# Kernel tuning notes

Measured on AMD Instinct MI355X. Metric: run time of the kernel, lower is better.

The kernel has to match this reference:

```python
import jax, jax.numpy as jnp
import numpy as np

NODE_DIM = 256
EDGE_IN = 128
EDGE_OUT = 128
BIAS_DIM = NODE_DIM // 2          # node_dilation = 2
HIDDEN = BIAS_DIM * 2 + EDGE_IN   # 384
B, N = 1, 512


def setup_inputs() -> dict:
    key = jax.random.key(0)
    ks = jax.random.split(key, 12)
    s = lambda fi, fo: 1.0 / np.sqrt(fi)
    return {
        "node_embed": jax.random.normal(ks[0], (B, N, NODE_DIM), jnp.float32),
        "edge_embed": jax.random.normal(ks[1], (B, N, N, EDGE_IN), jnp.float32),
        "w_init": jax.random.normal(ks[2], (NODE_DIM, BIAS_DIM), jnp.float32) * s(NODE_DIM, BIAS_DIM),
        "b_init": jnp.zeros((BIAS_DIM,), jnp.float32),
        "w_t0": jax.random.normal(ks[3], (HIDDEN, HIDDEN), jnp.float32) * s(HIDDEN, HIDDEN),
        "b_t0": jnp.zeros((HIDDEN,), jnp.float32),
        "w_t1": jax.random.normal(ks[4], (HIDDEN, HIDDEN), jnp.float32) * s(HIDDEN, HIDDEN),
        "b_t1": jnp.zeros((HIDDEN,), jnp.float32),
        "w_fin": jax.random.normal(ks[5], (HIDDEN, EDGE_OUT), jnp.float32) * 0.02,
        "b_fin": jnp.zeros((EDGE_OUT,), jnp.float32),
        "ln_g": jnp.ones((EDGE_OUT,), jnp.float32),
        "ln_b": jnp.zeros((EDGE_OUT,), jnp.float32),
    }


def _layer_norm(x, g, b, eps=1e-5):
    mu = jnp.mean(x, axis=-1, keepdims=True)
    var = jnp.mean(jnp.square(x - mu), axis=-1, keepdims=True)
    return (x - mu) * jax.lax.rsqrt(var + eps) * g + b


def reference(node_embed, edge_embed, w_init, b_init, w_t0, b_t0, w_t1, b_t1,
              w_fin, b_fin, ln_g, ln_b):
    b, n, _ = node_embed.shape
    # initial node projection: [B, N, BIAS_DIM]
    nb = node_embed @ w_init + b_init
    # edge_bias = concat(tile over j, tile over i): [B, N, N, 2*BIAS_DIM]
    bias_i = jnp.broadcast_to(nb[:, :, None, :], (b, n, n, nb.shape[-1]))
    bias_j = jnp.broadcast_to(nb[:, None, :, :], (b, n, n, nb.shape[-1]))
    h = jnp.concatenate([edge_embed, bias_i, bias_j], axis=-1)  # [B,N,N,HIDDEN]
    t = jax.nn.relu(h @ w_t0 + b_t0)
    t = jax.nn.relu(t @ w_t1 + b_t1)
    # residual + final linear + LayerNorm
    out = (t + h) @ w_fin + b_fin
    return _layer_norm(out, ln_g, ln_b)
```

## Files before the change

### kernel.cpp

```cpp
#include <hip/hip_runtime.h>


typedef short sv8 __attribute__((ext_vector_type(8)));
typedef float f32x4 __attribute__((ext_vector_type(4)));

union F8U { float4 v4[2]; float f[8]; };

__device__ __forceinline__ void async_cp16(const void* g, void* l) {
  __builtin_amdgcn_global_load_lds(
      (const __attribute__((address_space(1))) void*)g,
      (__attribute__((address_space(3))) void*)l, 16, 0, 0);
}

__device__ __forceinline__ void split8(const float* v, sv8& hi, sv8& lo) {
#pragma unroll
  for (int i = 0; i < 8; i++) {
    unsigned u = __float_as_uint(v[i]);
    hi[i] = (short)(u >> 16);
    float fl = v[i] - __uint_as_float(u & 0xFFFF0000u);
    lo[i] = (short)(__float_as_uint(fl) >> 16);
  }
}

__global__ void node_proj(const float* __restrict__ node,
                          const float* __restrict__ w,
                          const float* __restrict__ b,
                          float* __restrict__ nb) {
  __shared__ float sn[256];
  int i = blockIdx.x;
  int t = threadIdx.x;
  sn[t] = node[i * 256 + t];
  sn[t + 128] = node[i * 256 + t + 128];
  __syncthreads();
  float acc = b[t];
  for (int k = 0; k < 256; k++) acc += sn[k] * w[k * 128 + t];
  nb[i * 128 + t] = acc;
}

__global__ void pq_proj(const float* __restrict__ nb,
                        const float* __restrict__ w0,
                        const float* __restrict__ b0,
                        float* __restrict__ Pb, float* __restrict__ Qm) {
  __shared__ float sn[128];
  const int j = blockIdx.x, t = threadIdx.x;
  if (t < 128) sn[t] = nb[j * 128 + t];
  __syncthreads();
  float ap = b0[t], aq = 0.0f;
  for (int k = 0; k < 128; k++) {
    const float nk = sn[k];
    ap += nk * w0[(128 + k) * 384 + t];
    aq += nk * w0[(256 + k) * 384 + t];
  }
  Pb[j * 384 + t] = ap;
  Qm[j * 384 + t] = aq;
}

__global__ void pack_b(const float* __restrict__ W, int N, int NKT,
                       float* __restrict__ dst) {
  const int nt = blockIdx.x, kt = blockIdx.y, l = threadIdx.x;
  const int n = nt * 16 + (l & 15);
  const int k0 = kt * 32 + ((l >> 4) * 8);
  float v[8];
#pragma unroll
  for (int i = 0; i < 8; i++) v[i] = W[(size_t)(k0 + i) * N + n];
  sv8 hi, lo;
  split8(v, hi, lo);
  char* base = (char*)dst + (size_t)((nt * NKT + kt) * 2) * 1024;
  *(sv8*)(base + l * 16) = hi;
  *(sv8*)(base + 1024 + l * 16) = lo;
}

__device__ __forceinline__ void stage_e(const float* E, long mblk, int kt,
                                        char* dst, int wid, int lane) {
#pragma unroll
  for (int q = 0; q < 2; q++) {
    int c = wid * 2 + q;
    int row = c * 8 + (lane >> 3);
    int kb = ((lane & 7) * 16) ^ ((row & 7) << 4);
    const char* src =
        (const char*)E + (size_t)(mblk + row) * 512 + (size_t)kt * 128 + kb;
    async_cp16(src, dst + c * 1024);
  }
}

template <int PW>
__device__ __forceinline__ void stage_apk(const float* Apk, long mt0, int NKT,
                                          int kt, char* dst, int wid,
                                          int lane) {
#pragma unroll
  for (int q = 0; q < PW; q++) {
    int idx = wid * PW + q;
    int mt = idx >> 1, sp = idx & 1;
    const char* src = (const char*)Apk +
                      (size_t)(((mt0 + mt) * NKT + kt) * 2 + sp) * 1024 +
                      lane * 16;
    async_cp16(src, dst + idx * 1024);
  }
}

template <int PW>
__device__ __forceinline__ void stage_bpk(const float* Bpk, int NKT, int kt,
                                          char* dst, int wid, int lane) {
#pragma unroll
  for (int q = 0; q < PW; q++) {
    int idx = wid * PW + q;
    int nt = idx >> 1, sp = idx & 1;
    const char* src = (const char*)Bpk +
                      (size_t)((nt * NKT + kt) * 2 + sp) * 1024 + lane * 16;
    async_cp16(src, dst + idx * 1024);
  }
}

#define MFMA __builtin_amdgcn_mfma_f32_16x16x32_bf16

__global__ __launch_bounds__(512, 2) void gemm0_k(
    const float* __restrict__ E, const float* __restrict__ W0pk,
    const float* __restrict__ Pb, const float* __restrict__ Qm,
    float* __restrict__ C0pk, long m0) {
  __shared__ __align__(16) char sm[135168];
  const int t = threadIdx.x, lane = t & 63, wid = t >> 6;
  const int rb = wid >> 2, cb = wid & 3;
  const long mblk = m0 + (long)blockIdx.x * 128;
  const int i_node = (int)(mblk >> 9);
  float* sPb = (float*)(sm + 131072);
  if (t < 96)
    *(float4*)(sPb + t * 4) = *(const float4*)(Pb + i_node * 384 + t * 4);

  f32x4 acc[4][6] = {};

  stage_e(E, mblk, 0, sm, wid, lane);
  stage_bpk<6>(W0pk, 4, 0, sm + 32768, wid, lane);
  __syncthreads();

  for (int kt = 0; kt < 4; kt++) {
    const int buf = kt & 1;
    if (kt < 3) {
      stage_e(E, mblk, kt + 1, sm + (buf ^ 1) * 16384, wid, lane);
      stage_bpk<6>(W0pk, 4, kt + 1, sm + 32768 + (buf ^ 1) * 49152, wid, lane);
    }
    const char* sA = sm + buf * 16384;
    const char* sB = sm + 32768 + buf * 49152;
    sv8 ah[4], al[4], bh[6], bl[6];
#pragma unroll
    for (int rt = 0; rt < 4; rt++) {
      int row = rb * 64 + rt * 16 + (lane & 15);
      int c0 = (lane >> 4) * 32;
      F8U v;
      v.v4[0] = *(const float4*)(sA + row * 128 + (c0 ^ ((row & 7) << 4)));
      v.v4[1] =
          *(const float4*)(sA + row * 128 + ((c0 + 16) ^ ((row & 7) << 4)));
      split8(v.f, ah[rt], al[rt]);
    }
#pragma unroll
    for (int nt = 0; nt < 6; nt++) {
      int gnt = cb * 6 + nt;
      bh[nt] = *(const sv8*)(sB + gnt * 2048 + lane * 16);
      bl[nt] = *(const sv8*)(sB + gnt * 2048 + 1024 + lane * 16);
    }
#pragma unroll
    for (int rt = 0; rt < 4; rt++)
#pragma unroll
      for (int nt = 0; nt < 6; nt++) {
        acc[rt][nt] = MFMA(ah[rt], bh[nt], acc[rt][nt], 0, 0, 0);
        acc[rt][nt] = MFMA(ah[rt], bl[nt], acc[rt][nt], 0, 0, 0);
        acc[rt][nt] = MFMA(al[rt], bh[nt], acc[rt][nt], 0, 0, 0);
      }
    __syncthreads();
  }

  float* scr = (float*)(sm + wid * 16384);
  const long mrow0 = mblk + rb * 64;
#pragma unroll
  for (int h = 0; h < 2; h++) {
#pragma unroll
    for (int rt = 0; rt < 4; rt++)
#pragma unroll
      for (int ntl = 0; ntl < 3; ntl++) {
        int nt = h * 3 + ntl;
#pragma unroll
        for (int rg = 0; rg < 4; rg++) {
          int row = rt * 16 + (lane >> 4) * 4 + rg;
          scr[row * 52 + ntl * 16 + (lane & 15)] = acc[rt][nt][rg];
        }
      }
#pragma unroll
    for (int q = 0; q < 6; q++) {
      const int row = lane;
      const int colg = cb * 96 + h * 48 + q * 8;
      F8U v;
      v.v4[0] = *(float4*)(scr + row * 52 + q * 8);
      v.v4[1] = *(float4*)(scr + row * 52 + q * 8 + 4);
      const long m = mrow0 + row;
      const int j = (int)(m & 511);
      F8U qv;
      qv.v4[0] = *(const float4*)(Qm + (size_t)j * 384 + colg);
      qv.v4[1] = *(const float4*)(Qm + (size_t)j * 384 + colg + 4);
#pragma unroll
      for (int i = 0; i < 8; i++)
        v.f[i] = fmaxf(v.f[i] + sPb[colg + i] + qv.f[i], 0.0f);
      sv8 hi, lo;
      split8(v.f, hi, lo);
      const int rowb = rb * 64 + row;
      const long mt = (long)blockIdx.x * 8 + (rowb >> 4);
      const int lane2 = (rowb & 15) | (((colg >> 3) & 3) << 4);
      char* base = (char*)C0pk + (size_t)((mt * 12 + (colg >> 5)) * 2) * 1024;
      *(sv8*)(base + lane2 * 16) = hi;
      *(sv8*)(base + 1024 + lane2 * 16) = lo;
    }
  }
}

__global__ __launch_bounds__(512, 2) void gemm1_k(
    const float* __restrict__ C0pk, const float* __restrict__ W1pk,
    const float* __restrict__ b1, const float* __restrict__ E,
    const float* __restrict__ nb, float* __restrict__ A2pk, long m0) {
  __shared__ __align__(16) char sm[135168];
  const int t = threadIdx.x, lane = t & 63, wid = t >> 6;
  const int rb = wid >> 2, cb = wid & 3;
  const long mblk = m0 + (long)blockIdx.x * 128;
  const int i_node = (int)(mblk >> 9);
  float* sB1 = (float*)(sm + 131072);
  float* snbi = (float*)(sm + 131072 + 1536);
  if (t < 96) *(float4*)(sB1 + t * 4) = *(const float4*)(b1 + t * 4);
  if (t < 32)
    *(float4*)(snbi + t * 4) = *(const float4*)(nb + i_node * 128 + t * 4);

  f32x4 acc[4][6] = {};

  const long mt0 = (long)blockIdx.x * 8;
  stage_apk<2>(C0pk, mt0, 12, 0, sm, wid, lane);
  stage_bpk<6>(W1pk, 12, 0, sm + 32768, wid, lane);
  __syncthreads();

  for (int kt = 0; kt < 12; kt++) {
    const int buf = kt & 1;
    if (kt < 11) {
      stage_apk<2>(C0pk, mt0, 12, kt + 1, sm + (buf ^ 1) * 16384, wid, lane);
      stage_bpk<6>(W1pk, 12, kt + 1, sm + 32768 + (buf ^ 1) * 49152, wid,
                   lane);
    }
    const char* sA = sm + buf * 16384;
    const char* sB = sm + 32768 + buf * 49152;
    sv8 ah[4], al[4], bh[6], bl[6];
#pragma unroll
    for (int rt = 0; rt < 4; rt++) {
      int mtl = rb * 4 + rt;
      ah[rt] = *(const sv8*)(sA + mtl * 2048 + lane * 16);
      al[rt] = *(const sv8*)(sA + mtl * 2048 + 1024 + lane * 16);
    }
#pragma unroll
    for (int nt = 0; nt < 6; nt++) {
      int gnt = cb * 6 + nt;
      bh[nt] = *(const sv8*)(sB + gnt * 2048 + lane * 16);
      bl[nt] = *(const sv8*)(sB + gnt * 2048 + 1024 + lane * 16);
    }
#pragma unroll
    for (int rt = 0; rt < 4; rt++)
#pragma unroll
      for (int nt = 0; nt < 6; nt++) {
        acc[rt][nt] = MFMA(ah[rt], bh[nt], acc[rt][nt], 0, 0, 0);
        acc[rt][nt] = MFMA(ah[rt], bl[nt], acc[rt][nt], 0, 0, 0);
        acc[rt][nt] = MFMA(al[rt], bh[nt], acc[rt][nt], 0, 0, 0);
      }
    __syncthreads();
  }

  float* scr = (float*)(sm + wid * 16384);
  const long mrow0 = mblk + rb * 64;
#pragma unroll
  for (int h = 0; h < 2; h++) {
#pragma unroll
    for (int rt = 0; rt < 4; rt++)
#pragma unroll
      for (int ntl = 0; ntl < 3; ntl++) {
        int nt = h * 3 + ntl;
#pragma unroll
        for (int rg = 0; rg < 4; rg++) {
          int row = rt * 16 + (lane >> 4) * 4 + rg;
          scr[row * 52 + ntl * 16 + (lane & 15)] = acc[rt][nt][rg];
        }
      }
#pragma unroll
    for (int q = 0; q < 6; q++) {
      const int row = lane;
      const int colg = cb * 96 + h * 48 + q * 8;
      F8U v;
      v.v4[0] = *(float4*)(scr + row * 52 + q * 8);
      v.v4[1] = *(float4*)(scr + row * 52 + q * 8 + 4);
      const long m = mrow0 + row;
      const int j = (int)(m & 511);
      F8U hv;
      if (colg < 128) {
        hv.v4[0] = *(const float4*)(E + (size_t)m * 128 + colg);
        hv.v4[1] = *(const float4*)(E + (size_t)m * 128 + colg + 4);
      } else if (colg < 256) {
        hv.v4[0] = *(const float4*)(snbi + (colg - 128));
        hv.v4[1] = *(const float4*)(snbi + (colg - 128) + 4);
      } else {
        hv.v4[0] = *(const float4*)(nb + (size_t)j * 128 + (colg - 256));
        hv.v4[1] = *(const float4*)(nb + (size_t)j * 128 + (colg - 256) + 4);
      }
#pragma unroll
      for (int i = 0; i < 8; i++)
        v.f[i] = fmaxf(v.f[i] + sB1[colg + i], 0.0f) + hv.f[i];
      sv8 hi, lo;
      split8(v.f, hi, lo);
      const int rowb = rb * 64 + row;
      const long mt = (long)blockIdx.x * 8 + (rowb >> 4);
      const int lane2 = (rowb & 15) | (((colg >> 3) & 3) << 4);
      char* base = (char*)A2pk + (size_t)((mt * 12 + (colg >> 5)) * 2) * 1024;
      *(sv8*)(base + lane2 * 16) = hi;
      *(sv8*)(base + 1024 + lane2 * 16) = lo;
    }
  }
}

__global__ __launch_bounds__(256, 1) void gemmF_k(
    const float* __restrict__ A2pk, const float* __restrict__ Wfpk,
    const float* __restrict__ bfin, const float* __restrict__ lng,
    const float* __restrict__ lnb, float* __restrict__ out, long m0) {
  __shared__ __align__(16) char sm[135168];
  const int t = threadIdx.x, lane = t & 63, wid = t >> 6;
  const int rb = wid >> 1, cb = wid & 1;
  const long mblk = m0 + (long)blockIdx.x * 128;
  float* rep = (float*)(sm + 65536);
  float* sG = (float*)(sm + 133120);
  float* sB = sG + 128;
  float* sBf = sG + 256;
  if (t < 128) {
    sG[t] = lng[t];
    sB[t] = lnb[t];
    sBf[t] = bfin[t];
  }

  f32x4 acc[4][4] = {};
  const long mt0 = (long)blockIdx.x * 8;
  stage_apk<4>(A2pk, mt0, 12, 0, sm, wid, lane);
  stage_bpk<4>(Wfpk, 12, 0, sm + 32768, wid, lane);
  __syncthreads();

  for (int kt = 0; kt < 12; kt++) {
    const int buf = kt & 1;
    if (kt < 11) {
      stage_apk<4>(A2pk, mt0, 12, kt + 1, sm + (buf ^ 1) * 16384, wid, lane);
      stage_bpk<4>(Wfpk, 12, kt + 1, sm + 32768 + (buf ^ 1) * 16384, wid,
                   lane);
    }
    const char* sA = sm + buf * 16384;
    const char* sBt = sm + 32768 + buf * 16384;
    sv8 ah[4], al[4], bh[4], bl[4];
#pragma unroll
    for (int rt = 0; rt < 4; rt++) {
      int mtl = rb * 4 + rt;
      ah[rt] = *(const sv8*)(sA + mtl * 2048 + lane * 16);
      al[rt] = *(const sv8*)(sA + mtl * 2048 + 1024 + lane * 16);
    }
#pragma unroll
    for (int nt = 0; nt < 4; nt++) {
      int gnt = cb * 4 + nt;
      bh[nt] = *(const sv8*)(sBt + gnt * 2048 + lane * 16);
      bl[nt] = *(const sv8*)(sBt + gnt * 2048 + 1024 + lane * 16);
    }
#pragma unroll
    for (int rt = 0; rt < 4; rt++)
#pragma unroll
      for (int nt = 0; nt < 4; nt++) {
        acc[rt][nt] = MFMA(ah[rt], bh[nt], acc[rt][nt], 0, 0, 0);
        acc[rt][nt] = MFMA(ah[rt], bl[nt], acc[rt][nt], 0, 0, 0);
        acc[rt][nt] = MFMA(al[rt], bh[nt], acc[rt][nt], 0, 0, 0);
      }
    __syncthreads();
  }

#pragma unroll
  for (int rt = 0; rt < 4; rt++)
#pragma unroll
    for (int nt = 0; nt < 4; nt++)
#pragma unroll
      for (int rg = 0; rg < 4; rg++) {
        int row = rb * 64 + rt * 16 + (lane >> 4) * 4 + rg;
        int col = cb * 64 + nt * 16 + (lane & 15);
        rep[row * 132 + col] = acc[rt][nt][rg] + sBf[col];
      }
  __syncthreads();

  {
    const int row = t >> 1, hf = t & 1;
    float* rp = rep + row * 132 + hf * 64;
    float s = 0.0f, qq = 0.0f;
#pragma unroll
    for (int q = 0; q < 16; q++) {
      float4 v = *(float4*)(rp + q * 4);
      s += v.x + v.y + v.z + v.w;
      qq += v.x * v.x + v.y * v.y + v.z * v.z + v.w * v.w;
    }
    s += __shfl_xor(s, 1);
    qq += __shfl_xor(qq, 1);
    const float mu = s * (1.0f / 128.0f);
    const float var = qq * (1.0f / 128.0f) - mu * mu;
    const float rstd = rsqrtf(var + 1e-5f);
    float* op = out + (size_t)(mblk + row) * 128 + hf * 64;
#pragma unroll
    for (int q = 0; q < 16; q++) {
      float4 v = *(float4*)(rp + q * 4);
      const int c = hf * 64 + q * 4;
      float4 o;
      o.x = (v.x - mu) * rstd * sG[c + 0] + sB[c + 0];
      o.y = (v.y - mu) * rstd * sG[c + 1] + sB[c + 1];
      o.z = (v.z - mu) * rstd * sG[c + 2] + sB[c + 2];
      o.w = (v.w - mu) * rstd * sG[c + 3] + sB[c + 3];
      *(float4*)(op + q * 4) = o;
    }
  }
}

#define ROWS 32
#define PF 388
#define TM 8
union F4 { float4 v; float f[4]; };
union F2 { float2 v; float f[2]; };

__device__ __forceinline__ void stage_tile7(const float* __restrict__ g,
                                            float* l, int nchunk, int t) {
  const int lane = t & 63, wid = t >> 6;
  for (int c = wid; c < nchunk; c += 8)
    async_cp16(g + c * 256 + lane * 4, l + c * 256);
}

__device__ __forceinline__ void trunk_tile7(const float* __restrict__ src,
                                            int koff,
                                            const float* __restrict__ wt,
                                            int cA, int cB, int mr,
                                            float acc[TM][3]) {
  for (int kk = 0; kk < 16; kk += 4) {
    F4 a[TM];
#pragma unroll
    for (int r = 0; r < TM; r++)
      a[r].v = *(const float4*)(src + (mr + r) * PF + koff + kk);
#pragma unroll
    for (int ks = 0; ks < 4; ks++) {
      const float* wrow = wt + (kk + ks) * 384;
      F2 w2;
      w2.v = *(const float2*)(wrow + cA);
      const float w1 = wrow[cB];
#pragma unroll
      for (int r = 0; r < TM; r++) {
        const float ak = a[r].f[ks];
        acc[r][0] += ak * w2.f[0];
        acc[r][1] += ak * w2.f[1];
        acc[r][2] += ak * w1;
      }
    }
  }
}

__global__ __launch_bounds__(512, 1) void edge_fused_r7(
    const float* __restrict__ edge, const float* __restrict__ nbf,
    const float* __restrict__ Pb, const float* __restrict__ Qm,
    const float* __restrict__ w0, const float* __restrict__ w1,
    const float* __restrict__ b1v, const float* __restrict__ wf,
    const float* __restrict__ bfin, const float* __restrict__ lng,
    const float* __restrict__ lnb, float* __restrict__ out) {
  __shared__ __align__(16) float Abuf[ROWS * PF];
  __shared__ __align__(16) float Bbuf[ROWS * PF];
  __shared__ __align__(16) float Wt[2][16 * 384];
  __shared__ __align__(16) float snbi[128];

  const int t = threadIdx.x;
  const int ct = t & 63;
  const int g = t >> 8;
  const int mr = ((t >> 6) & 3) * TM;
  const int cA = g * 192 + 2 * ct;
  const int cB = g * 192 + 128 + ct;
  const int r0 = blockIdx.x * ROWS;
  const int i_node = r0 >> 9, j0 = r0 & 511;

  {
    const int row = t >> 4, q = t & 15;
    const float* ep = edge + (size_t)(r0 + row) * 128 + q * 8;
    float* ap = Abuf + row * PF + q * 8;
    *(float4*)(ap + 0) = *(const float4*)(ep + 0);
    *(float4*)(ap + 4) = *(const float4*)(ep + 4);
  }
  if (t < 32)
    *(float4*)(snbi + t * 4) = *(const float4*)(nbf + i_node * 128 + t * 4);

  stage_tile7(w0, Wt[0], 24, t);

  float acc[TM][3];
  {
    const float* pr = Pb + i_node * 384;
    F2 p2;
    p2.v = *(const float2*)(pr + cA);
    const float p1 = pr[cB];
#pragma unroll
    for (int r = 0; r < TM; r++) {
      const float* qr = Qm + (size_t)(j0 + mr + r) * 384;
      F2 q2;
      q2.v = *(const float2*)(qr + cA);
      acc[r][0] = p2.f[0] + q2.f[0];
      acc[r][1] = p2.f[1] + q2.f[1];
      acc[r][2] = p1 + qr[cB];
    }
  }

  for (int kt = 0; kt < 8; kt++) {
    __syncthreads();
    if (kt < 7) stage_tile7(w0 + (kt + 1) * 6144, Wt[(kt + 1) & 1], 24, t);
    trunk_tile7(Abuf, kt * 16, Wt[kt & 1], cA, cB, mr, acc);
  }

  stage_tile7(w1, Wt[0], 24, t);
#pragma unroll
  for (int r = 0; r < TM; r++) {
    float* dr = Bbuf + (mr + r) * PF;
    F2 e2;
    e2.f[0] = fmaxf(acc[r][0], 0.0f);
    e2.f[1] = fmaxf(acc[r][1], 0.0f);
    *(float2*)(dr + cA) = e2.v;
    dr[cB] = fmaxf(acc[r][2], 0.0f);
  }

  {
    F2 c2;
    c2.v = *(const float2*)(b1v + cA);
    const float c1 = b1v[cB];
#pragma unroll
    for (int r = 0; r < TM; r++) {
      acc[r][0] = c2.f[0];
      acc[r][1] = c2.f[1];
      acc[r][2] = c1;
    }
  }

  for (int kt = 0; kt < 24; kt++) {
    __syncthreads();
    if (kt < 23) stage_tile7(w1 + (kt + 1) * 6144, Wt[(kt + 1) & 1], 24, t);
    trunk_tile7(Bbuf, kt * 16, Wt[kt & 1], cA, cB, mr, acc);
  }

  stage_tile7(wf, Wt[0], 16, t);

#pragma unroll
  for (int r = 0; r < TM; r++) {
    const int row = mr + r;
    float* dr = Abuf + row * PF;
    const float* njr = nbf + (size_t)(j0 + row) * 128;
#pragma unroll
    for (int c = 0; c < 2; c++) {
      const int col = cA + c;
      const float hv = (col < 128) ? dr[col]
                     : (col < 256) ? snbi[col - 128]
                                   : njr[col - 256];
      dr[col] = fmaxf(acc[r][c], 0.0f) + hv;
    }
    {
      const float hv = (cB < 128) ? dr[cB]
                     : (cB < 256) ? snbi[cB - 128]
                                  : njr[cB - 256];
      dr[cB] = fmaxf(acc[r][2], 0.0f) + hv;
    }
  }

  const int mrF = (t >> 6) * 4;
  float af[4][2];
  {
    F2 b2;
    b2.v = *(const float2*)(bfin + ct * 2);
#pragma unroll
    for (int r = 0; r < 4; r++) {
      af[r][0] = b2.f[0];
      af[r][1] = b2.f[1];
    }
  }
  for (int ft = 0; ft < 12; ft++) {
    __syncthreads();
    if (ft < 11) stage_tile7(wf + (ft + 1) * 4096, Wt[(ft + 1) & 1], 16, t);
    const float* wtc = Wt[ft & 1] + ct * 2;
    const int koff = ft * 32;
    for (int kk = 0; kk < 32; kk += 4) {
      F4 a[4];
#pragma unroll
      for (int r = 0; r < 4; r++)
        a[r].v = *(const float4*)(Abuf + (mrF + r) * PF + koff + kk);
#pragma unroll
      for (int ks = 0; ks < 4; ks++) {
        F2 wv;
        wv.v = *(const float2*)(wtc + (kk + ks) * 128);
#pragma unroll
        for (int r = 0; r < 4; r++) {
          const float ak = a[r].f[ks];
          af[r][0] += ak * wv.f[0];
          af[r][1] += ak * wv.f[1];
        }
      }
    }
  }

  {
    F2 g2, bb2;
    g2.v = *(const float2*)(lng + ct * 2);
    bb2.v = *(const float2*)(lnb + ct * 2);
#pragma unroll
    for (int r = 0; r < 4; r++) {
      float s = af[r][0] + af[r][1];
      float q = af[r][0] * af[r][0] + af[r][1] * af[r][1];
#pragma unroll
      for (int off = 1; off <= 32; off <<= 1) {
        s += __shfl_xor(s, off);
        q += __shfl_xor(q, off);
      }
      const float mu = s * (1.0f / 128.0f);
      const float var = q * (1.0f / 128.0f) - mu * mu;
      const float rstd = rsqrtf(var + 1e-5f);
      F2 o;
      o.f[0] = (af[r][0] - mu) * rstd * g2.f[0] + bb2.f[0];
      o.f[1] = (af[r][1] - mu) * rstd * g2.f[1] + bb2.f[1];
      *(float2*)(out + (size_t)(r0 + mrF + r) * 128 + ct * 2) = o.v;
    }
  }
}

extern "C" void kernel_launch(void* const* d_in, const int* in_sizes, int n_in,
                              void* d_out, int out_size, void* d_ws,
                              size_t ws_size, hipStream_t stream) {
  const float* node   = (const float*)d_in[0];
  const float* edge   = (const float*)d_in[1];
  const float* w_init = (const float*)d_in[2];
  const float* b_init = (const float*)d_in[3];
  const float* w_t0   = (const float*)d_in[4];
  const float* b_t0   = (const float*)d_in[5];
  const float* w_t1   = (const float*)d_in[6];
  const float* b_t1   = (const float*)d_in[7];
  const float* w_fin  = (const float*)d_in[8];
  const float* b_fin  = (const float*)d_in[9];
  const float* ln_g   = (const float*)d_in[10];
  const float* ln_b   = (const float*)d_in[11];
  float* out = (float*)d_out;
  float* ws = (float*)d_ws;

  float* nbw  = ws;
  float* Pb   = ws + 65536;
  float* Qm   = ws + 262144;
  float* W0pk = ws + 458752;
  float* W1pk = ws + 507904;
  float* Wfpk = ws + 655360;
  float* C0pk = ws + 704512;

  node_proj<<<512, 128, 0, stream>>>(node, w_init, b_init, nbw);
  pq_proj<<<512, 384, 0, stream>>>(nbw, w_t0, b_t0, Pb, Qm);

  int S = 0;
  long stripe_rows = 0;
  for (int s = 8; s <= 256; s *= 2) {
    long sr = 262144L / s;
    size_t need = (704512ull + 2ull * (size_t)sr * 384ull) * 4ull;
    if (need <= ws_size) { S = s; stripe_rows = sr; break; }
  }

  if (S == 0) {
    edge_fused_r7<<<8192, 512, 0, stream>>>(edge, nbw, Pb, Qm, w_t0, w_t1,
                                            b_t1, w_fin, b_fin, ln_g, ln_b,
                                            out);
    return;
  }

  float* A2pk = C0pk + (size_t)stripe_rows * 384;
  const int blocks = (int)(stripe_rows / 128);

  pack_b<<<dim3(24, 4), 64, 0, stream>>>(w_t0, 384, 4, W0pk);
  pack_b<<<dim3(24, 12), 64, 0, stream>>>(w_t1, 384, 12, W1pk);
  pack_b<<<dim3(8, 12), 64, 0, stream>>>(w_fin, 128, 12, Wfpk);

  for (int s = 0; s < S; s++) {
    const long m0 = (long)s * stripe_rows;
    gemm0_k<<<blocks, 512, 0, stream>>>(edge, W0pk, Pb, Qm, C0pk, m0);
    gemm1_k<<<blocks, 512, 0, stream>>>(C0pk, W1pk, b_t1, edge, nbw, A2pk, m0);
    gemmF_k<<<blocks, 256, 0, stream>>>(A2pk, Wfpk, b_fin, ln_g, ln_b, out,
                                        m0);
  }
}
```

Before: 939.5 us.

## Shrink LDS footprint of trunk GEMM kernels to raise occupancy

Cuts shared memory in gemm0/gemm1 from about 132KB to 80KB by single-buffering the weight tile (reloaded after an extra barrier) and shrinking the epilogue scratch to 32-row halves. Bias and node-projection vectors are now read from global memory instead of LDS. gemmF drops its 64KB row staging buffer and computes LayerNorm statistics in registers with shuffles plus a small LDS reduction. Launch bounds are raised so more blocks can share a CU. In exchange the weight loads are no longer overlapped with compute, each k-step gets an extra barrier, and gemmF's output stores are scalar rather than float4.

```diff
diff --git a/kernel.cpp b/kernel.cpp
--- a/kernel.cpp
+++ b/kernel.cpp
@@ -113,18 +113,15 @@
 
 #define MFMA __builtin_amdgcn_mfma_f32_16x16x32_bf16
 
-__global__ __launch_bounds__(512, 2) void gemm0_k(
+__global__ __launch_bounds__(512, 4) void gemm0_k(
     const float* __restrict__ E, const float* __restrict__ W0pk,
     const float* __restrict__ Pb, const float* __restrict__ Qm,
     float* __restrict__ C0pk, long m0) {
-  __shared__ __align__(16) char sm[135168];
+  __shared__ __align__(16) char sm[81920];
   const int t = threadIdx.x, lane = t & 63, wid = t >> 6;
   const int rb = wid >> 2, cb = wid & 3;
   const long mblk = m0 + (long)blockIdx.x * 128;
   const int i_node = (int)(mblk >> 9);
-  float* sPb = (float*)(sm + 131072);
-  if (t < 96)
-    *(float4*)(sPb + t * 4) = *(const float4*)(Pb + i_node * 384 + t * 4);
 
   f32x4 acc[4][6] = {};
 
@@ -133,13 +130,10 @@
   __syncthreads();
 
   for (int kt = 0; kt < 4; kt++) {
-    const int buf = kt & 1;
-    if (kt < 3) {
-      stage_e(E, mblk, kt + 1, sm + (buf ^ 1) * 16384, wid, lane);
-      stage_bpk<6>(W0pk, 4, kt + 1, sm + 32768 + (buf ^ 1) * 49152, wid, lane);
-    }
-    const char* sA = sm + buf * 16384;
-    const char* sB = sm + 32768 + buf * 49152;
+    if (kt < 3) stage_e(E, mblk, kt + 1, sm + ((kt + 1) & 1) * 16384, wid, lane);
+
+    const char* sA = sm + (kt & 1) * 16384;
+    const char* sB = sm + 32768;
     sv8 ah[4], al[4], bh[6], bl[6];
 #pragma unroll
     for (int rt = 0; rt < 4; rt++) {
@@ -166,81 +160,83 @@
         acc[rt][nt] = MFMA(al[rt], bh[nt], acc[rt][nt], 0, 0, 0);
       }
     __syncthreads();
-  }
-
-  float* scr = (float*)(sm + wid * 16384);
-  const long mrow0 = mblk + rb * 64;
+    if (kt < 3) {
+      stage_bpk<6>(W0pk, 4, kt + 1, sm + 32768, wid, lane);
+      __syncthreads();
+    }
+  }
+
+  float* scr = (float*)(sm + wid * 10240);
+  const int row32r = lane & 31;
 #pragma unroll
   for (int h = 0; h < 2; h++) {
 #pragma unroll
-    for (int rt = 0; rt < 4; rt++)
-#pragma unroll
-      for (int ntl = 0; ntl < 3; ntl++) {
-        int nt = h * 3 + ntl;
-#pragma unroll
-        for (int rg = 0; rg < 4; rg++) {
-          int row = rt * 16 + (lane >> 4) * 4 + rg;
-          scr[row * 52 + ntl * 16 + (lane & 15)] = acc[rt][nt][rg];
-        }
-      }
-#pragma unroll
-    for (int q = 0; q < 6; q++) {
-      const int row = lane;
-      const int colg = cb * 96 + h * 48 + q * 8;
-      F8U v;
-      v.v4[0] = *(float4*)(scr + row * 52 + q * 8);
-      v.v4[1] = *(float4*)(scr + row * 52 + q * 8 + 4);
-      const long m = mrow0 + row;
+    for (int rh = 0; rh < 2; rh++) {
+#pragma unroll
+      for (int rt2 = 0; rt2 < 2; rt2++)
+#pragma unroll
+        for (int ntl = 0; ntl < 3; ntl++)
+#pragma unroll
+          for (int rg = 0; rg < 4; rg++) {
+            int row32 = rt2 * 16 + (lane >> 4) * 4 + rg;
+            scr[row32 * 52 + ntl * 16 + (lane & 15)] =
+                acc[rh * 2 + rt2][h * 3 + ntl][rg];
+          }
+      const int rowb = rb * 64 + rh * 32 + row32r;
+      const long m = mblk + rowb;
       const int j = (int)(m & 511);
-      F8U qv;
-      qv.v4[0] = *(const float4*)(Qm + (size_t)j * 384 + colg);
-      qv.v4[1] = *(const float4*)(Qm + (size_t)j * 384 + colg + 4);
-#pragma unroll
-      for (int i = 0; i < 8; i++)
-        v.f[i] = fmaxf(v.f[i] + sPb[colg + i] + qv.f[i], 0.0f);
-      sv8 hi, lo;
-      split8(v.f, hi, lo);
-      const int rowb = rb * 64 + row;
-      const long mt = (long)blockIdx.x * 8 + (rowb >> 4);
-      const int lane2 = (rowb & 15) | (((colg >> 3) & 3) << 4);
-      char* base = (char*)C0pk + (size_t)((mt * 12 + (colg >> 5)) * 2) * 1024;
-      *(sv8*)(base + lane2 * 16) = hi;
-      *(sv8*)(base + 1024 + lane2 * 16) = lo;
-    }
-  }
-}
-
-__global__ __launch_bounds__(512, 2) void gemm1_k(
+#pragma unroll
+      for (int qq = 0; qq < 3; qq++) {
+        const int cloc = ((lane >> 5) * 3 + qq) * 8;
+        const int colg = cb * 96 + h * 48 + cloc;
+        F8U v;
+        v.v4[0] = *(float4*)(scr + row32r * 52 + cloc);
+        v.v4[1] = *(float4*)(scr + row32r * 52 + cloc + 4);
+        F8U pv, qv;
+        pv.v4[0] = *(const float4*)(Pb + (size_t)i_node * 384 + colg);
+        pv.v4[1] = *(const float4*)(Pb + (size_t)i_node * 384 + colg + 4);
+        qv.v4[0] = *(const float4*)(Qm + (size_t)j * 384 + colg);
+        qv.v4[1] = *(const float4*)(Qm + (size_t)j * 384 + colg + 4);
+#pragma unroll
+        for (int i = 0; i < 8; i++)
+          v.f[i] = fmaxf(v.f[i] + pv.f[i] + qv.f[i], 0.0f);
+        sv8 hi, lo;
+        split8(v.f, hi, lo);
+        const long mt = (long)blockIdx.x * 8 + (rowb >> 4);
+        const int lane2 = (rowb & 15) | (((colg >> 3) & 3) << 4);
+        char* base =
+            (char*)C0pk + (size_t)((mt * 12 + (colg >> 5)) * 2) * 1024;
+        *(sv8*)(base + lane2 * 16) = hi;
+        *(sv8*)(base + 1024 + lane2 * 16) = lo;
+      }
+    }
+  }
+}
+
+__global__ __launch_bounds__(512, 4) void gemm1_k(
     const float* __restrict__ C0pk, const float* __restrict__ W1pk,
     const float* __restrict__ b1, const float* __restrict__ E,
     const float* __restrict__ nb, float* __restrict__ A2pk, long m0) {
-  __shared__ __align__(16) char sm[135168];
+  __shared__ __align__(16) char sm[81920];
   const int t = threadIdx.x, lane = t & 63, wid = t >> 6;
   const int rb = wid >> 2, cb = wid & 3;
   const long mblk = m0 + (long)blockIdx.x * 128;
   const int i_node = (int)(mblk >> 9);
-  float* sB1 = (float*)(sm + 131072);
-  float* snbi = (float*)(sm + 131072 + 1536);
-  if (t < 96) *(float4*)(sB1 + t * 4) = *(const float4*)(b1 + t * 4);
-  if (t < 32)
-    *(float4*)(snbi + t * 4) = *(const float4*)(nb + i_node * 128 + t * 4);
+  const long mt0 = (long)blockIdx.x * 8;
 
   f32x4 acc[4][6] = {};
 
-  const long mt0 = (long)blockIdx.x * 8;
   stage_apk<2>(C0pk, mt0, 12, 0, sm, wid, lane);
   stage_bpk<6>(W1pk, 12, 0, sm + 32768, wid, lane);
   __syncthreads();
 
   for (int kt = 0; kt < 12; kt++) {
-    const int buf = kt & 1;
-    if (kt < 11) {
-      stage_apk<2>(C0pk, mt0, 12, kt + 1, sm + (buf ^ 1) * 16384, wid, lane);
-      stage_bpk<6>(W1pk, 12, kt + 1, sm + 32768 + (buf ^ 1) * 49152, wid,
+    if (kt < 11)
+      stage_apk<2>(C0pk, mt0, 12, kt + 1, sm + ((kt + 1) & 1) * 16384, wid,
                    lane);
-    }
-    const char* sA = sm + buf * 16384;
-    const char* sB = sm + 32768 + buf * 49152;
+
+    const char* sA = sm + (kt & 1) * 16384;
+    const char* sB = sm + 32768;
     sv8 ah[4], al[4], bh[6], bl[6];
 #pragma unroll
     for (int rt = 0; rt < 4; rt++) {
@@ -263,70 +259,80 @@
         acc[rt][nt] = MFMA(al[rt], bh[nt], acc[rt][nt], 0, 0, 0);
       }
     __syncthreads();
-  }
-
-  float* scr = (float*)(sm + wid * 16384);
-  const long mrow0 = mblk + rb * 64;
+    if (kt < 11) {
+      stage_bpk<6>(W1pk, 12, kt + 1, sm + 32768, wid, lane);
+      __syncthreads();
+    }
+  }
+
+  float* scr = (float*)(sm + wid * 10240);
+  const int row32r = lane & 31;
 #pragma unroll
   for (int h = 0; h < 2; h++) {
 #pragma unroll
-    for (int rt = 0; rt < 4; rt++)
-#pragma unroll
-      for (int ntl = 0; ntl < 3; ntl++) {
-        int nt = h * 3 + ntl;
-#pragma unroll
-        for (int rg = 0; rg < 4; rg++) {
-          int row = rt * 16 + (lane >> 4) * 4 + rg;
-          scr[row * 52 + ntl * 16 + (lane & 15)] = acc[rt][nt][rg];
+    for (int rh = 0; rh < 2; rh++) {
+#pragma unroll
+      for (int rt2 = 0; rt2 < 2; rt2++)
+#pragma unroll
+        for (int ntl = 0; ntl < 3; ntl++)
+#pragma unroll
+          for (int rg = 0; rg < 4; rg++) {
+            int row32 = rt2 * 16 + (lane >> 4) * 4 + rg;
+            scr[row32 * 52 + ntl * 16 + (lane & 15)] =
+                acc[rh * 2 + rt2][h * 3 + ntl][rg];
+          }
+      const int rowb = rb * 64 + rh * 32 + row32r;
+      const long m = mblk + rowb;
+      const int j = (int)(m & 511);
+#pragma unroll
+      for (int qq = 0; qq < 3; qq++) {
+        const int cloc = ((lane >> 5) * 3 + qq) * 8;
+        const int colg = cb * 96 + h * 48 + cloc;
+        F8U v;
+        v.v4[0] = *(float4*)(scr + row32r * 52 + cloc);
+        v.v4[1] = *(float4*)(scr + row32r * 52 + cloc + 4);
+        F8U bv, hv;
+        bv.v4[0] = *(const float4*)(b1 + colg);
+        bv.v4[1] = *(const float4*)(b1 + colg + 4);
+        if (colg < 128) {
+          hv.v4[0] = *(const float4*)(E + (size_t)m * 128 + colg);
+          hv.v4[1] = *(const float4*)(E + (size_t)m * 128 + colg + 4);
+        } else if (colg < 256) {
+          hv.v4[0] = *(const float4*)(nb + (size_t)i_node * 128 + (colg - 128));
+          hv.v4[1] =
+              *(const float4*)(nb + (size_t)i_node * 128 + (colg - 128) + 4);
+        } else {
+          hv.v4[0] = *(const float4*)(nb + (size_t)j * 128 + (colg - 256));
+          hv.v4[1] = *(const float4*)(nb + (size_t)j * 128 + (colg - 256) + 4);
         }
-      }
-#pragma unroll
-    for (int q = 0; q < 6; q++) {
-      const int row = lane;
-      const int colg = cb * 96 + h * 48 + q * 8;
-      F8U v;
-      v.v4[0] = *(float4*)(scr + row * 52 + q * 8);
-      v.v4[1] = *(float4*)(scr + row * 52 + q * 8 + 4);
-      const long m = mrow0 + row;
-      const int j = (int)(m & 511);
-      F8U hv;
-      if (colg < 128) {
-        hv.v4[0] = *(const float4*)(E + (size_t)m * 128 + colg);
-        hv.v4[1] = *(const float4*)(E + (size_t)m * 128 + colg + 4);
-      } else if (colg < 256) {
-        hv.v4[0] = *(const float4*)(snbi + (colg - 128));
-        hv.v4[1] = *(const float4*)(snbi + (colg - 128) + 4);
-      } else {
-        hv.v4[0] = *(const float4*)(nb + (size_t)j * 128 + (colg - 256));
-        hv.v4[1] = *(const float4*)(nb + (size_t)j * 128 + (colg - 256) + 4);
-      }
-#pragma unroll
-      for (int i = 0; i < 8; i++)
-        v.f[i] = fmaxf(v.f[i] + sB1[colg + i], 0.0f) + hv.f[i];
-      sv8 hi, lo;
-      split8(v.f, hi, lo);
-      const int rowb = rb * 64 + row;
-      const long mt = (long)blockIdx.x * 8 + (rowb >> 4);
-      const int lane2 = (rowb & 15) | (((colg >> 3) & 3) << 4);
-      char* base = (char*)A2pk + (size_t)((mt * 12 + (colg >> 5)) * 2) * 1024;
-      *(sv8*)(base + lane2 * 16) = hi;
-      *(sv8*)(base + 1024 + lane2 * 16) = lo;
-    }
-  }
-}
-
-__global__ __launch_bounds__(256, 1) void gemmF_k(
+#pragma unroll
+        for (int i = 0; i < 8; i++)
+          v.f[i] = fmaxf(v.f[i] + bv.f[i], 0.0f) + hv.f[i];
+        sv8 hi, lo;
+        split8(v.f, hi, lo);
+        const long mt = (long)blockIdx.x * 8 + (rowb >> 4);
+        const int lane2 = (rowb & 15) | (((colg >> 3) & 3) << 4);
+        char* base =
+            (char*)A2pk + (size_t)((mt * 12 + (colg >> 5)) * 2) * 1024;
+        *(sv8*)(base + lane2 * 16) = hi;
+        *(sv8*)(base + 1024 + lane2 * 16) = lo;
+      }
+    }
+  }
+}
+
+__global__ __launch_bounds__(256, 2) void gemmF_k(
     const float* __restrict__ A2pk, const float* __restrict__ Wfpk,
     const float* __restrict__ bfin, const float* __restrict__ lng,
     const float* __restrict__ lnb, float* __restrict__ out, long m0) {
-  __shared__ __align__(16) char sm[135168];
+  __shared__ __align__(16) char sm[69632];
   const int t = threadIdx.x, lane = t & 63, wid = t >> 6;
   const int rb = wid >> 1, cb = wid & 1;
   const long mblk = m0 + (long)blockIdx.x * 128;
-  float* rep = (float*)(sm + 65536);
-  float* sG = (float*)(sm + 133120);
+  float* sG = (float*)(sm + 65536);
   float* sB = sG + 128;
   float* sBf = sG + 256;
+  float* sLN = sG + 384;
   if (t < 128) {
     sG[t] = lng[t];
     sB[t] = lnb[t];
@@ -375,43 +381,46 @@
 #pragma unroll
   for (int rt = 0; rt < 4; rt++)
 #pragma unroll
-    for (int nt = 0; nt < 4; nt++)
-#pragma unroll
-      for (int rg = 0; rg < 4; rg++) {
-        int row = rb * 64 + rt * 16 + (lane >> 4) * 4 + rg;
-        int col = cb * 64 + nt * 16 + (lane & 15);
-        rep[row * 132 + col] = acc[rt][nt][rg] + sBf[col];
-      }
+    for (int rg = 0; rg < 4; rg++) {
+      float s = 0.0f, q = 0.0f;
+#pragma unroll
+      for (int nt = 0; nt < 4; nt++) {
+        const int col = cb * 64 + nt * 16 + (lane & 15);
+        const float v = acc[rt][nt][rg] + sBf[col];
+        s += v;
+        q += v * v;
+      }
+#pragma unroll
+      for (int off = 1; off <= 8; off <<= 1) {
+        s += __shfl_xor(s, off);
+        q += __shfl_xor(q, off);
+      }
+      const int row = rb * 64 + rt * 16 + (lane >> 4) * 4 + rg;
+      if ((lane & 15) == 0) {
+        sLN[row * 4 + cb * 2 + 0] = s;
+        sLN[row * 4 + cb * 2 + 1] = q;
+      }
+    }
   __syncthreads();
 
-  {
-    const int row = t >> 1, hf = t & 1;
-    float* rp = rep + row * 132 + hf * 64;
-    float s = 0.0f, qq = 0.0f;
-#pragma unroll
-    for (int q = 0; q < 16; q++) {
-      float4 v = *(float4*)(rp + q * 4);
-      s += v.x + v.y + v.z + v.w;
-      qq += v.x * v.x + v.y * v.y + v.z * v.z + v.w * v.w;
-    }
-    s += __shfl_xor(s, 1);
-    qq += __shfl_xor(qq, 1);
-    const float mu = s * (1.0f / 128.0f);
-    const float var = qq * (1.0f / 128.0f) - mu * mu;
-    const float rstd = rsqrtf(var + 1e-5f);
-    float* op = out + (size_t)(mblk + row) * 128 + hf * 64;
-#pragma unroll
-    for (int q = 0; q < 16; q++) {
-      float4 v = *(float4*)(rp + q * 4);
-      const int c = hf * 64 + q * 4;
-      float4 o;
-      o.x = (v.x - mu) * rstd * sG[c + 0] + sB[c + 0];
-      o.y = (v.y - mu) * rstd * sG[c + 1] + sB[c + 1];
-      o.z = (v.z - mu) * rstd * sG[c + 2] + sB[c + 2];
-      o.w = (v.w - mu) * rstd * sG[c + 3] + sB[c + 3];
-      *(float4*)(op + q * 4) = o;
-    }
-  }
+#pragma unroll
+  for (int rt = 0; rt < 4; rt++)
+#pragma unroll
+    for (int rg = 0; rg < 4; rg++) {
+      const int row = rb * 64 + rt * 16 + (lane >> 4) * 4 + rg;
+      const float s = sLN[row * 4 + 0] + sLN[row * 4 + 2];
+      const float q = sLN[row * 4 + 1] + sLN[row * 4 + 3];
+      const float mu = s * (1.0f / 128.0f);
+      const float var = q * (1.0f / 128.0f) - mu * mu;
+      const float rstd = rsqrtf(var + 1e-5f);
+      float* op = out + (size_t)(mblk + row) * 128;
+#pragma unroll
+      for (int nt = 0; nt < 4; nt++) {
+        const int col = cb * 64 + nt * 16 + (lane & 15);
+        const float v = acc[rt][nt][rg] + sBf[col];
+        op[col] = (v - mu) * rstd * sG[col] + sB[col];
+      }
+    }
 }
 
 #define ROWS 32
```

Measured after the change: 2.188 ms. 2.33x slower.
